# Kernel optimization log

Measured on AMD Instinct MI355X. Metric: run time of the kernel, lower is better.

Reference implementation:

```python
import jax, jax.numpy as jnp
import numpy as np

B, T, D, H = 256, 256, 512, 8
HD = D // H  # 64


def _rope_tables(t, hd):
    pos = jnp.arange(t, dtype=jnp.float32)
    inv_freq = 1.0 / (10000.0 ** (jnp.arange(0, hd, 2, dtype=jnp.float32) / hd))
    ang = pos[:, None] * inv_freq[None, :]            # (T, hd/2)
    cos = jnp.repeat(jnp.cos(ang), 2, axis=-1)        # (T, hd) interleaved pairs
    sin = jnp.repeat(jnp.sin(ang), 2, axis=-1)
    return cos, sin


def setup_inputs() -> dict:
    key = jax.random.key(0)
    k1, k2, k3 = jax.random.split(key, 3)
    x = jax.random.normal(k1, (B, T, D), dtype=jnp.float32)
    cos, sin = _rope_tables(T, HD)
    Wqkv = jax.random.normal(k2, (3 * D, D), dtype=jnp.float32) * 0.02
    Wout = jax.random.normal(k3, (D, D), dtype=jnp.float32) * 0.02
    return {"x": x, "cos": cos, "sin": sin, "Wqkv": Wqkv, "Wout": Wout}


def _apply_rope(x, cos, sin):
    # x: (B, T, H, hd); cos/sin: (T, hd)
    x1 = x[..., 0::2]
    x2 = x[..., 1::2]
    rot = jnp.stack((-x2, x1), axis=-1).reshape(x.shape)  # interleaved rotate
    return x * cos[None, :, None, :] + rot * sin[None, :, None, :]


def reference(x, cos, sin, Wqkv, Wout):
    b, t, d = x.shape
    qkv = (x @ Wqkv.T).reshape(b, t, 3, H, HD)
    q, k, v = qkv[:, :, 0], qkv[:, :, 1], qkv[:, :, 2]   # (B, T, H, hd)
    q = _apply_rope(q, cos[:t], sin[:t])
    k = _apply_rope(k, cos[:t], sin[:t])
    q = q.transpose(0, 2, 1, 3)  # (B, H, T, hd)
    k = k.transpose(0, 2, 1, 3)
    v = v.transpose(0, 2, 1, 3)
    scale = 1.0 / jnp.sqrt(jnp.float32(HD))
    scores = jnp.einsum('bhqd,bhkd->bhqk', q, k) * scale
    causal = jnp.arange(t)[:, None] >= jnp.arange(t)[None, :]  # (T, T)
    scores = jnp.where(causal[None, None], scores, jnp.finfo(scores.dtype).min)
    att = jax.nn.softmax(scores, axis=-1)
    out = jnp.einsum('bhqk,bhkd->bhqd', att, v)          # (B, H, T, hd)
    out = out.transpose(0, 2, 1, 3).reshape(b, t, d)
    return out @ Wout.T
```

## Files before the change

kernel.cpp:

```cpp
#include <hip/hip_runtime.h>

typedef float floatx4 __attribute__((ext_vector_type(4)));
typedef short short8 __attribute__((ext_vector_type(8)));
typedef unsigned short ushort_t;

#define AS1 __attribute__((address_space(1)))
#define AS3 __attribute__((address_space(3)))

__device__ __forceinline__ void gload_lds16(const ushort_t* g, ushort_t* l) {
    __builtin_amdgcn_global_load_lds((const AS1 unsigned int*)g, (AS3 unsigned int*)l, 16, 0, 0);
}

__device__ __forceinline__ ushort_t f2bf(float f) {
    union { float f; unsigned u; } v; v.f = f;
    unsigned r = v.u + 0x7FFFu + ((v.u >> 16) & 1u);
    return (ushort_t)(r >> 16);
}

#define KDIM 512
#define LOG2E 1.44269504f

#define XB_OFF   0ull
#define ATT_OFF  0ull
#define WQKV_OFF 33554432ull
#define WOUT_OFF 34340864ull
#define QB_OFF   34603008ull
#define KB_OFF   68157440ull
#define VB_OFF   101711872ull

__global__ __launch_bounds__(256) void convert_k(
    const float* __restrict__ x, const float* __restrict__ wqkv,
    const float* __restrict__ wout, ushort_t* __restrict__ dst)
{
    size_t i = (size_t)blockIdx.x * 256 + threadIdx.x;
    size_t e = i * 4;
    const float* s; size_t o;
    if (e < 33554432ull)      { s = x;    o = e; }
    else if (e < 34340864ull) { s = wqkv; o = e - 33554432ull; }
    else                      { s = wout; o = e - 34340864ull; }
    float4 v = *(const float4*)(s + o);
    ushort4 r;
    r.x = f2bf(v.x); r.y = f2bf(v.y); r.z = f2bf(v.z); r.w = f2bf(v.w);
    *(ushort4*)(dst + e) = r;
}

template <int EPI>
__global__ __launch_bounds__(256, 3) void gemm_bt(
    const ushort_t* __restrict__ A, const ushort_t* __restrict__ Bw,
    float* __restrict__ Cf,
    ushort_t* __restrict__ qout, ushort_t* __restrict__ kout, ushort_t* __restrict__ vout,
    const float* __restrict__ cosT, const float* __restrict__ sinT)
{
    __shared__ __align__(16) ushort_t As[128 * 64];
    __shared__ __align__(16) ushort_t Bs[128 * 64];
    const int bn = blockIdx.x, bm = blockIdx.y;
    const int tid = threadIdx.x;
    const int lane = tid & 63, wave = tid >> 6;
    const int wm = wave & 1, wn = wave >> 1;
    const int quad = lane >> 4, l16 = lane & 15;

    const ushort_t* Ag = A + (size_t)bm * 128 * KDIM;
    const ushort_t* Bg = Bw + (size_t)bn * 128 * KDIM;

    floatx4 acc[4][4] = {};

    for (int k0 = 0; k0 < KDIM; k0 += 64) {
#pragma unroll
        for (int ii = 0; ii < 4; ii++) {
            int e8 = ii * 256 + tid;
            int row = e8 >> 3, col = (e8 & 7) << 3;
            gload_lds16(Ag + row * KDIM + k0 + col, &As[e8 * 8]);
            gload_lds16(Bg + row * KDIM + k0 + col, &Bs[e8 * 8]);
        }
        __syncthreads();
#pragma unroll
        for (int kk = 0; kk < 2; kk++) {
            short8 af[4], bf[4];
#pragma unroll
            for (int mi = 0; mi < 4; mi++)
                af[mi] = *(const short8*)&As[(wm * 64 + mi * 16 + l16) * 64 + kk * 32 + quad * 8];
#pragma unroll
            for (int ni = 0; ni < 4; ni++)
                bf[ni] = *(const short8*)&Bs[(wn * 64 + ni * 16 + l16) * 64 + kk * 32 + quad * 8];
#pragma unroll
            for (int mi = 0; mi < 4; mi++)
#pragma unroll
                for (int ni = 0; ni < 4; ni++)
                    acc[mi][ni] = __builtin_amdgcn_mfma_f32_16x16x32_bf16(
                        af[mi], bf[ni], acc[mi][ni], 0, 0, 0);
        }
        __syncthreads();
    }

    if constexpr (EPI == 1) {
        const int n_base = bn * 128 + wn * 64;
        const int qkv = n_base >> 9;
        ushort_t* dst = (qkv == 0) ? qout : (qkv == 1 ? kout : vout);
#pragma unroll
        for (int mi = 0; mi < 4; mi++) {
            const int m = bm * 128 + wm * 64 + mi * 16 + quad * 4;
#pragma unroll
            for (int ni = 0; ni < 4; ni++) {
                const int n = n_base + ni * 16 + l16;
                const int nw = n & 511, hd = n & 63;
#pragma unroll
                for (int r = 0; r < 4; r++) {
                    const int mm = m + r, t = mm & 255;
                    const size_t dsti = (size_t)mm * 512 + nw;
                    float val = acc[mi][ni][r];
                    if (qkv == 2) {
                        dst[dsti] = f2bf(val);
                    } else {
                        float partner = __shfl_xor(val, 1);
                        float c = cosT[t * 64 + hd], s = sinT[t * 64 + hd];
                        float o = val * c + ((hd & 1) ? partner : -partner) * s;
                        dst[dsti] = (qkv == 0) ? f2bf(o * 0.125f) : f2bf(o);
                    }
                }
            }
        }
    } else {
#pragma unroll
        for (int mi = 0; mi < 4; mi++) {
            const int m = bm * 128 + wm * 64 + mi * 16 + quad * 4;
#pragma unroll
            for (int ni = 0; ni < 4; ni++) {
                const int n = bn * 128 + wn * 64 + ni * 16 + l16;
#pragma unroll
                for (int r = 0; r < 4; r++)
                    Cf[(size_t)(m + r) * 512 + n] = acc[mi][ni][r];
            }
        }
    }
}

__global__ __launch_bounds__(256) void attn_k(
    const ushort_t* __restrict__ qb, const ushort_t* __restrict__ kb,
    const ushort_t* __restrict__ vb, ushort_t* __restrict__ attb)
{
    __shared__ __align__(16) ushort_t Ks[256 * 72];
    __shared__ __align__(16) ushort_t Vt[64 * 264];
    __shared__ __align__(16) ushort_t Ps[4 * 32 * 40];

    const int blk = blockIdx.x;
    const int qt = blk & 1, bh = blk >> 1;
    const int b = bh >> 3, h = bh & 7;
    const int tid = threadIdx.x, lane = tid & 63, w = tid >> 6;
    const int quad = lane >> 4, l16 = lane & 15;
    const int q0 = qt * 128;
    const int kend = q0 + 128;

    const ushort_t* Kg = kb + ((size_t)b * 256) * 512 + h * 64;
    const ushort_t* Vg = vb + ((size_t)b * 256) * 512 + h * 64;
    const ushort_t* Qg = qb + ((size_t)b * 256) * 512 + h * 64;

    for (int e8 = tid; e8 < kend * 8; e8 += 256) {
        int t = e8 >> 3, c = (e8 & 7) << 3;
        *(short8*)&Ks[t * 72 + c] = *(const short8*)&Kg[t * 512 + c];
        short8 vv = *(const short8*)&Vg[t * 512 + c];
#pragma unroll
        for (int j = 0; j < 8; j++) Vt[(c + j) * 264 + t] = ((const ushort_t*)&vv)[j];
    }
    __syncthreads();

    short8 qf[2][2];
#pragma unroll
    for (int mi = 0; mi < 2; mi++)
#pragma unroll
        for (int kk = 0; kk < 2; kk++)
            qf[mi][kk] = *(const short8*)&Qg[(size_t)(q0 + w * 32 + mi * 16 + l16) * 512 + kk * 32 + quad * 8];

    float lsum[2][4] = {};
    floatx4 o_[2][4] = {};

    ushort_t* Pw = &Ps[w * 32 * 40];
    const int ktdiag = qt * 4 + w;

    for (int kt = 0; kt <= ktdiag; kt++) {
        const bool diag = (kt == ktdiag);
        floatx4 s_[2][2] = {};
#pragma unroll
        for (int kk = 0; kk < 2; kk++) {
            short8 kf0 = *(const short8*)&Ks[(kt * 32 + l16) * 72 + kk * 32 + quad * 8];
            short8 kf1 = *(const short8*)&Ks[(kt * 32 + 16 + l16) * 72 + kk * 32 + quad * 8];
#pragma unroll
            for (int mi = 0; mi < 2; mi++) {
                s_[mi][0] = __builtin_amdgcn_mfma_f32_16x16x32_bf16(qf[mi][kk], kf0, s_[mi][0], 0, 0, 0);
                s_[mi][1] = __builtin_amdgcn_mfma_f32_16x16x32_bf16(qf[mi][kk], kf1, s_[mi][1], 0, 0, 0);
            }
        }
#pragma unroll
        for (int mi = 0; mi < 2; mi++) {
#pragma unroll
            for (int r = 0; r < 4; r++) {
                float p0 = exp2f(s_[mi][0][r] * LOG2E);
                float p1 = exp2f(s_[mi][1][r] * LOG2E);
                if (diag) {
                    const int rl = mi * 16 + quad * 4 + r;
                    if (l16 > rl)      p0 = 0.f;
                    if (l16 + 16 > rl) p1 = 0.f;
                }
                lsum[mi][r] += p0 + p1;
                const int rowL = mi * 16 + quad * 4 + r;
                Pw[rowL * 40 + l16] = f2bf(p0);
                Pw[rowL * 40 + 16 + l16] = f2bf(p1);
            }
        }
        __asm__ volatile("s_waitcnt lgkmcnt(0)" ::: "memory");
        short8 pf[2];
#pragma unroll
        for (int mi = 0; mi < 2; mi++)
            pf[mi] = *(const short8*)&Pw[(mi * 16 + l16) * 40 + quad * 8];
#pragma unroll
        for (int vni = 0; vni < 4; vni++) {
            short8 vf = *(const short8*)&Vt[(vni * 16 + l16) * 264 + kt * 32 + quad * 8];
#pragma unroll
            for (int mi = 0; mi < 2; mi++)
                o_[mi][vni] = __builtin_amdgcn_mfma_f32_16x16x32_bf16(pf[mi], vf, o_[mi][vni], 0, 0, 0);
        }
    }

#pragma unroll
    for (int mi = 0; mi < 2; mi++) {
#pragma unroll
        for (int r = 0; r < 4; r++) {
            float rs = lsum[mi][r];
            rs += __shfl_xor(rs, 1);
            rs += __shfl_xor(rs, 2);
            rs += __shfl_xor(rs, 4);
            rs += __shfl_xor(rs, 8);
            const float inv = 1.f / rs;
            const int t = q0 + w * 32 + mi * 16 + quad * 4 + r;
            const size_t base = ((size_t)(b * 256 + t)) * 512 + h * 64;
#pragma unroll
            for (int vni = 0; vni < 4; vni++)
                attb[base + vni * 16 + l16] = f2bf(o_[mi][vni][r] * inv);
        }
    }
}

extern "C" void kernel_launch(void* const* d_in, const int* in_sizes, int n_in,
                              void* d_out, int out_size, void* d_ws, size_t ws_size,
                              hipStream_t stream) {
    const float* x    = (const float*)d_in[0];
    const float* cosT = (const float*)d_in[1];
    const float* sinT = (const float*)d_in[2];
    const float* wqkv = (const float*)d_in[3];
    const float* wout = (const float*)d_in[4];
    float* out = (float*)d_out;
    ushort_t* ws = (ushort_t*)d_ws;

    ushort_t* xb    = ws + XB_OFF;
    ushort_t* wqkvb = ws + WQKV_OFF;
    ushort_t* woutb = ws + WOUT_OFF;
    ushort_t* qbp   = ws + QB_OFF;
    ushort_t* kbp   = ws + KB_OFF;
    ushort_t* vbp   = ws + VB_OFF;
    ushort_t* attb  = ws + ATT_OFF;

    convert_k<<<33792, 256, 0, stream>>>(x, wqkv, wout, ws);
    gemm_bt<1><<<dim3(12, 512), 256, 0, stream>>>(xb, wqkvb, nullptr, qbp, kbp, vbp, cosT, sinT);
    attn_k<<<4096, 256, 0, stream>>>(qbp, kbp, vbp, attb);
    gemm_bt<0><<<dim3(4, 512), 256, 0, stream>>>(attb, woutb, out, nullptr, nullptr, nullptr, nullptr, nullptr);
}
```

Measured before the change: 587.1 us.

## Stage GEMM epilogues through LDS, remap blocks per XCD, vectorize V transpose

Both GEMM epilogues now write their accumulators into shared memory first and then store to global memory with 16-byte vectorized row-contiguous writes, replacing the scattered 2- and 4-byte stores. The block index is remapped so that consecutive row tiles land on the same XCD, which should improve L2 reuse of A tiles. The V transpose in attention reads four rows at once and writes 8-byte vectors into the transposed LDS tile instead of single elements. The costs are extra syncthreads, a larger shared array that may reduce occupancy, and the cost of the LDS round trip.

```diff
diff --git a/kernel.cpp b/kernel.cpp
--- a/kernel.cpp
+++ b/kernel.cpp
@@ -2,6 +2,7 @@
 
 typedef float floatx4 __attribute__((ext_vector_type(4)));
 typedef short short8 __attribute__((ext_vector_type(8)));
+typedef short short4v __attribute__((ext_vector_type(4)));
 typedef unsigned short ushort_t;
 
 #define AS1 __attribute__((address_space(1)))
@@ -44,16 +45,22 @@
     *(ushort4*)(dst + e) = r;
 }
 
-template <int EPI>
+template <int EPI, int NB>
 __global__ __launch_bounds__(256, 3) void gemm_bt(
     const ushort_t* __restrict__ A, const ushort_t* __restrict__ Bw,
     float* __restrict__ Cf,
     ushort_t* __restrict__ qout, ushort_t* __restrict__ kout, ushort_t* __restrict__ vout,
     const float* __restrict__ cosT, const float* __restrict__ sinT)
 {
-    __shared__ __align__(16) ushort_t As[128 * 64];
-    __shared__ __align__(16) ushort_t Bs[128 * 64];
-    const int bn = blockIdx.x, bm = blockIdx.y;
+    __shared__ __align__(16) ushort_t SM[17408];
+    ushort_t* As = SM;
+    ushort_t* Bs = SM + 8192;
+
+    const int fl = blockIdx.x + blockIdx.y * NB;
+    const int xcd = fl & 7, s_ = fl >> 3;
+    const int bm = xcd * 64 + s_ / NB;
+    const int bn = s_ % NB;
+
     const int tid = threadIdx.x;
     const int lane = tid & 63, wave = tid >> 6;
     const int wm = wave & 1, wn = wave >> 1;
@@ -93,42 +100,65 @@
     }
 
     if constexpr (EPI == 1) {
-        const int n_base = bn * 128 + wn * 64;
-        const int qkv = n_base >> 9;
+        const int n_block = bn * 128;
+        const int qkv = n_block >> 9;
+        const int colbase = n_block & 511;
         ushort_t* dst = (qkv == 0) ? qout : (qkv == 1 ? kout : vout);
 #pragma unroll
         for (int mi = 0; mi < 4; mi++) {
-            const int m = bm * 128 + wm * 64 + mi * 16 + quad * 4;
+            const int rlb = wm * 64 + mi * 16 + quad * 4;
+            const int m = bm * 128 + rlb;
 #pragma unroll
             for (int ni = 0; ni < 4; ni++) {
-                const int n = n_base + ni * 16 + l16;
-                const int nw = n & 511, hd = n & 63;
+                const int cl = wn * 64 + ni * 16 + l16;
+                const int hd = cl & 63;
 #pragma unroll
                 for (int r = 0; r < 4; r++) {
-                    const int mm = m + r, t = mm & 255;
-                    const size_t dsti = (size_t)mm * 512 + nw;
                     float val = acc[mi][ni][r];
+                    ushort_t bf;
                     if (qkv == 2) {
-                        dst[dsti] = f2bf(val);
+                        bf = f2bf(val);
                     } else {
                         float partner = __shfl_xor(val, 1);
+                        const int t = (m + r) & 255;
                         float c = cosT[t * 64 + hd], s = sinT[t * 64 + hd];
                         float o = val * c + ((hd & 1) ? partner : -partner) * s;
-                        dst[dsti] = (qkv == 0) ? f2bf(o * 0.125f) : f2bf(o);
+                        bf = (qkv == 0) ? f2bf(o * 0.125f) : f2bf(o);
                     }
+                    SM[(rlb + r) * 136 + cl] = bf;
                 }
             }
         }
+        __syncthreads();
+#pragma unroll
+        for (int it = 0; it < 8; it++) {
+            int idx = it * 256 + tid;
+            int row = idx >> 4, ch = idx & 15;
+            short8 v = *(const short8*)&SM[row * 136 + ch * 8];
+            int mm = bm * 128 + row;
+            *(short8*)&dst[(size_t)mm * 512 + colbase + ch * 8] = v;
+        }
     } else {
+        float* Fs = (float*)SM;
 #pragma unroll
         for (int mi = 0; mi < 4; mi++) {
-            const int m = bm * 128 + wm * 64 + mi * 16 + quad * 4;
+            __syncthreads();
+            const int r32b = wm * 16 + quad * 4;
 #pragma unroll
             for (int ni = 0; ni < 4; ni++) {
-                const int n = bn * 128 + wn * 64 + ni * 16 + l16;
+                const int cl = wn * 64 + ni * 16 + l16;
 #pragma unroll
                 for (int r = 0; r < 4; r++)
-                    Cf[(size_t)(m + r) * 512 + n] = acc[mi][ni][r];
+                    Fs[(r32b + r) * 132 + cl] = acc[mi][ni][r];
+            }
+            __syncthreads();
+#pragma unroll
+            for (int it = 0; it < 4; it++) {
+                int idx = it * 256 + tid;
+                int row32 = idx >> 5, ch = idx & 31;
+                float4 v = *(const float4*)&Fs[row32 * 132 + ch * 4];
+                int mm = bm * 128 + (row32 >> 4) * 64 + mi * 16 + (row32 & 15);
+                *(float4*)&Cf[(size_t)mm * 512 + bn * 128 + ch * 4] = v;
             }
         }
     }
@@ -157,9 +187,18 @@
     for (int e8 = tid; e8 < kend * 8; e8 += 256) {
         int t = e8 >> 3, c = (e8 & 7) << 3;
         *(short8*)&Ks[t * 72 + c] = *(const short8*)&Kg[t * 512 + c];
-        short8 vv = *(const short8*)&Vg[t * 512 + c];
-#pragma unroll
-        for (int j = 0; j < 8; j++) Vt[(c + j) * 264 + t] = ((const ushort_t*)&vv)[j];
+    }
+    for (int it = tid; it < kend * 2; it += 256) {
+        int t4 = it >> 3, c = (it & 7) << 3, t = t4 * 4;
+        short8 r0 = *(const short8*)&Vg[(size_t)(t + 0) * 512 + c];
+        short8 r1 = *(const short8*)&Vg[(size_t)(t + 1) * 512 + c];
+        short8 r2 = *(const short8*)&Vg[(size_t)(t + 2) * 512 + c];
+        short8 r3 = *(const short8*)&Vg[(size_t)(t + 3) * 512 + c];
+#pragma unroll
+        for (int j = 0; j < 8; j++) {
+            short4v p; p[0] = r0[j]; p[1] = r1[j]; p[2] = r2[j]; p[3] = r3[j];
+            *(short4v*)&Vt[(c + j) * 264 + t] = p;
+        }
     }
     __syncthreads();
 
@@ -259,7 +298,7 @@
     ushort_t* attb  = ws + ATT_OFF;
 
     convert_k<<<33792, 256, 0, stream>>>(x, wqkv, wout, ws);
-    gemm_bt<1><<<dim3(12, 512), 256, 0, stream>>>(xb, wqkvb, nullptr, qbp, kbp, vbp, cosT, sinT);
+    gemm_bt<1, 12><<<dim3(12, 512), 256, 0, stream>>>(xb, wqkvb, nullptr, qbp, kbp, vbp, cosT, sinT);
     attn_k<<<4096, 256, 0, stream>>>(qbp, kbp, vbp, attb);
-    gemm_bt<0><<<dim3(4, 512), 256, 0, stream>>>(attb, woutb, out, nullptr, nullptr, nullptr, nullptr, nullptr);
-}
+    gemm_bt<0, 4><<<dim3(4, 512), 256, 0, stream>>>(attb, woutb, out, nullptr, nullptr, nullptr, nullptr, nullptr);
+}
```

Result: no change. 587.7 us (+0.1%).
